# Performance work log

Hardware: AMD Instinct MI355X
Metric: run time of the kernel (lower is better)

The kernel has to match this reference:

```python
import jax, jax.numpy as jnp
import numpy as np

ALPHA = 30.0  # init kwarg alpha
K = 16        # init kwarg k


def setup_inputs() -> dict:
    key = jax.random.key(0)
    k1, k2 = jax.random.split(key)
    x = jax.random.normal(k1, (4096, 1024), dtype=jnp.float32)
    # L2-normalize embeddings (standard for metric-learning losses) so
    # pairwise distances lie in [0, 2] and exp(alpha*(1-d)) is well-scaled.
    x = x / jnp.linalg.norm(x, axis=1, keepdims=True)
    t = jax.random.randint(k2, (4096,), 0, 64)
    return {"inputs": x, "targets": t}


def _knn_softmax(inputs, targets):
    n = inputs.shape[0]
    # pairwise euclidean distances, clamp(1e-12).sqrt as in euclidean_dist
    sq = jnp.sum(inputs * inputs, axis=1)
    dist = sq[:, None] + sq[None, :] - 2.0 * (inputs @ inputs.T)
    dist = jnp.sqrt(jnp.clip(dist, 1e-12))  # [n, n]

    eye = jnp.eye(n, dtype=bool)
    same = targets[:, None] == targets[None, :]
    pos_mask = same & ~eye        # same label, off-diagonal
    neg_mask = ~same              # different label (diag excluded automatically)

    # threshold = (K+1)-th smallest off-diagonal distance per row
    # (equals sorted(concat(pos_pair, neg_pair))[K] in the original)
    BIG = jnp.float32(1e30)
    thr = jnp.sort(jnp.where(eye, BIG, dist), axis=1)[:, K]  # [n]

    below = dist < thr[:, None]
    logits = jnp.exp(ALPHA * (1.0 - dist))  # exp(alpha*(1 - d)) per pair

    pos_below = pos_mask & below
    neg_below = neg_mask & below
    pos_logit = jnp.sum(jnp.where(pos_below, logits, 0.0), axis=1)
    neg_logit = jnp.sum(jnp.where(neg_below, logits, 0.0), axis=1)

    # fallback: if no positive neighbor below threshold, use the first
    # positive pair (masked_select returns row order -> smallest index)
    first_pos = jnp.argmax(pos_mask, axis=1)
    fb = jnp.take_along_axis(logits, first_pos[:, None], axis=1)[:, 0]
    has_pos_below = jnp.any(pos_below, axis=1)
    pos_logit = jnp.where(has_pos_below, pos_logit, fb)

    loss_i = -jnp.log(pos_logit / (pos_logit + neg_logit))  # [n]

    # rows with no positive or no negative pair are skipped in the original
    valid = jnp.any(pos_mask, axis=1) & jnp.any(neg_mask, axis=1)
    n_valid = jnp.sum(valid.astype(jnp.float32))
    loss = jnp.sum(jnp.where(valid, loss_i, 0.0)) / n_valid
    accuracy = jnp.sum((valid & (loss_i < 0.6)).astype(jnp.float32)) / n
    return loss, accuracy


def reference(inputs, targets):
    loss, accuracy = _knn_softmax(inputs, targets)
    return (loss, accuracy, 0.0, 0.0)
```

## Files before the change

### kernel.cpp

```cpp
#include <hip/hip_runtime.h>
#include <hip/hip_bf16.h>
#include <cfloat>
#include <climits>
#include <cstdint>

#define ALPHA 30.0f
#define KSEL 16
#define P0 1.368f
#define P0SQ (P0 * P0)
#define CAP 224
#define TCAP 512
#define BIGV 1e30f
#define NMAX 4096

typedef __attribute__((ext_vector_type(4))) float f32x4;
typedef __attribute__((ext_vector_type(8))) int i32x8;
typedef __attribute__((ext_vector_type(4))) int i32x4;

#define LDS_PTR(p) ((__attribute__((address_space(3))) uint32_t*)(p))
#define GLB_PTR(p) ((const __attribute__((address_space(1))) uint32_t*)(p))

__device__ inline float bfval(ushort u) {
    return __builtin_bit_cast(float, (uint32_t)u << 16);
}

__device__ inline float blockReduceSumF(float v, float* s) {
    for (int off = 32; off; off >>= 1) v += __shfl_down(v, off);
    int tid = threadIdx.x, wid = tid >> 6;
    if ((tid & 63) == 0) s[wid] = v;
    __syncthreads();
    float r;
    if (tid == 0) { r = s[0] + s[1] + s[2] + s[3]; s[0] = r; }
    __syncthreads();
    r = s[0];
    __syncthreads();
    return r;
}

__device__ inline int blockReduceSumI(int v, int* s) {
    for (int off = 32; off; off >>= 1) v += __shfl_down(v, off);
    int tid = threadIdx.x, wid = tid >> 6;
    if ((tid & 63) == 0) s[wid] = v;
    __syncthreads();
    int r;
    if (tid == 0) { r = s[0] + s[1] + s[2] + s[3]; s[0] = r; }
    __syncthreads();
    r = s[0];
    __syncthreads();
    return r;
}

__device__ inline int blockReduceMaxI(int v, int* s) {
    for (int off = 32; off; off >>= 1) v = max(v, __shfl_down(v, off));
    int tid = threadIdx.x, wid = tid >> 6;
    if ((tid & 63) == 0) s[wid] = v;
    __syncthreads();
    int r;
    if (tid == 0) { r = max(max(s[0], s[1]), max(s[2], s[3])); s[0] = r; }
    __syncthreads();
    r = s[0];
    __syncthreads();
    return r;
}

__global__ __launch_bounds__(256) void prep_kernel(const float* __restrict__ X,
                                                   ushort* __restrict__ Xbf,
                                                   uint32_t* __restrict__ Xb8,
                                                   float* __restrict__ sq,
                                                   const int* __restrict__ targets,
                                                   int* __restrict__ f1,
                                                   int* __restrict__ f2,
                                                   int* __restrict__ lcnt,
                                                   int* __restrict__ cntArr,
                                                   int* __restrict__ needFB,
                                                   int D, int N) {
    __shared__ float sw[4];
    __shared__ int s1[4], s2[4], sc[4];
    int tid = threadIdx.x;
    int wid = tid >> 6;

    if (blockIdx.x >= (unsigned)N) {
        int lbl = blockIdx.x - N;
        int a1 = INT_MAX, a2 = INT_MAX, c = 0;
        for (int j = tid; j < N; j += 256) {
            if (targets[j] == lbl) {
                ++c;
                if (j < a1) { a2 = a1; a1 = j; }
                else if (j < a2) a2 = j;
            }
        }
        for (int off = 32; off; off >>= 1) {
            int b1 = __shfl_down(a1, off), b2 = __shfl_down(a2, off), bc = __shfl_down(c, off);
            int m1 = min(a1, b1);
            int m2 = min(max(a1, b1), min(a2, b2));
            a1 = m1; a2 = m2; c += bc;
        }
        if ((tid & 63) == 0) { s1[wid] = a1; s2[wid] = a2; sc[wid] = c; }
        __syncthreads();
        if (tid == 0) {
            int r1 = s1[0], r2 = s2[0], rc = sc[0];
            for (int w = 1; w < 4; ++w) {
                int m1 = min(r1, s1[w]);
                int m2 = min(max(r1, s1[w]), min(r2, s2[w]));
                r1 = m1; r2 = m2; rc += sc[w];
            }
            f1[lbl] = r1; f2[lbl] = r2; lcnt[lbl] = rc;
        }
        return;
    }

    int row = blockIdx.x;
    if (tid == 0) { cntArr[row] = 0; needFB[row] = 0; }
    const float4* xr = reinterpret_cast<const float4*>(X + (size_t)row * D);
    ushort4* xo = reinterpret_cast<ushort4*>(Xbf + (size_t)row * D);
    uint32_t* x8o = Xb8 + (size_t)row * (D / 4);
    float s = 0.f;
    for (int c = tid; c < D / 4; c += 256) {
        float4 v = xr[c];
        s += v.x * v.x + v.y * v.y + v.z * v.z + v.w * v.w;
        ushort4 o;
        uint32_t b;
        b = __builtin_bit_cast(uint32_t, v.x); o.x = (ushort)((b + 0x7FFF + ((b >> 16) & 1)) >> 16);
        b = __builtin_bit_cast(uint32_t, v.y); o.y = (ushort)((b + 0x7FFF + ((b >> 16) & 1)) >> 16);
        b = __builtin_bit_cast(uint32_t, v.z); o.z = (ushort)((b + 0x7FFF + ((b >> 16) & 1)) >> 16);
        b = __builtin_bit_cast(uint32_t, v.w); o.w = (ushort)((b + 0x7FFF + ((b >> 16) & 1)) >> 16);
        xo[c] = o;
        int pk = __builtin_amdgcn_cvt_pk_fp8_f32(v.x * 16.f, v.y * 16.f, 0, false);
        pk = __builtin_amdgcn_cvt_pk_fp8_f32(v.z * 16.f, v.w * 16.f, pk, true);
        x8o[c] = (uint32_t)pk;
    }
    for (int off = 32; off; off >>= 1) s += __shfl_down(s, off);
    if ((tid & 63) == 0) sw[wid] = s;
    __syncthreads();
    if (tid == 0) sq[row] = sw[0] + sw[1] + sw[2] + sw[3];
}

#define GBM 128
#define GBK 128
__global__ __launch_bounds__(256) void distgemm_mfma(const uint8_t* __restrict__ Xb8,
                                                     const float* __restrict__ sq,
                                                     float2* __restrict__ cand,
                                                     int* __restrict__ cntArr,
                                                     int* __restrict__ needFB,
                                                     int N, int D) {
    if (blockIdx.x < blockIdx.y) return;
    __shared__ uint8_t As[GBM * GBK];
    __shared__ uint8_t Bs[GBM * GBK];
    __shared__ float2 tlist[TCAP];
    __shared__ int s_cnt;

    int by = blockIdx.y, bx = blockIdx.x;
    bool diag = (bx == by);

    int tid = threadIdx.x;
    int lane = tid & 63;
    int wave = tid >> 6;
    int waveR = wave >> 1;
    int waveC = wave & 1;

    int rowBase = by * GBM;
    int colBase = bx * GBM;

    if (tid == 0) s_cnt = 0;

    f32x4 acc[4][4];
#pragma unroll
    for (int m = 0; m < 4; ++m)
#pragma unroll
        for (int n2 = 0; n2 < 4; ++n2) {
            f32x4 z = {0.f, 0.f, 0.f, 0.f};
            acc[m][n2] = z;
        }

    int srow = lane >> 3;
    int sgb = ((lane & 7) << 4) ^ (srow << 4);
    auto STAGE = [&](int k0) {
#pragma unroll
        for (int p = 0; p < 4; ++p) {
            int c = wave * 4 + p;
            int r = c * 8 + srow;
            const uint8_t* gA = Xb8 + (size_t)(rowBase + r) * D + k0 + sgb;
            const uint8_t* gB = Xb8 + (size_t)(colBase + r) * D + k0 + sgb;
            __builtin_amdgcn_global_load_lds(GLB_PTR(gA), LDS_PTR(&As[c * 1024]), 16, 0, 0);
            __builtin_amdgcn_global_load_lds(GLB_PTR(gB), LDS_PTR(&Bs[c * 1024]), 16, 0, 0);
        }
    };

    int l15 = lane & 15;
    int kq32 = (lane >> 4) * 32;
    int rswz = (l15 & 7) << 4;
    int nt = D / GBK;

    for (int t = 0; t < nt; ++t) {
        STAGE(t * GBK);
        __syncthreads();

        i32x8 bF[4];
#pragma unroll
        for (int n2 = 0; n2 < 4; ++n2) {
            int brl = waveC * 64 + n2 * 16 + l15;
            const uint8_t* base = Bs + brl * 128;
            i32x4 lo = *reinterpret_cast<const i32x4*>(base + ((kq32) ^ rswz));
            i32x4 hi = *reinterpret_cast<const i32x4*>(base + ((kq32 + 16) ^ rswz));
            i32x8 f = {lo[0], lo[1], lo[2], lo[3], hi[0], hi[1], hi[2], hi[3]};
            bF[n2] = f;
        }
        __builtin_amdgcn_s_setprio(1);
#pragma unroll
        for (int m = 0; m < 4; ++m) {
            int arl = waveR * 64 + m * 16 + l15;
            const uint8_t* base = As + arl * 128;
            i32x4 lo = *reinterpret_cast<const i32x4*>(base + ((kq32) ^ rswz));
            i32x4 hi = *reinterpret_cast<const i32x4*>(base + ((kq32 + 16) ^ rswz));
            i32x8 aF = {lo[0], lo[1], lo[2], lo[3], hi[0], hi[1], hi[2], hi[3]};
#pragma unroll
            for (int n2 = 0; n2 < 4; ++n2)
                acc[m][n2] = __builtin_amdgcn_mfma_scale_f32_16x16x128_f8f6f4(
                    aF, bF[n2], acc[m][n2], 0, 0, 0, 0x7F, 0, 0x7F);
        }
        __builtin_amdgcn_s_setprio(0);
        __syncthreads();
    }

    int cr = (lane >> 4) * 4;
    int cc = lane & 15;
    unsigned long long lmask_lt = (1ull << lane) - 1ull;
#pragma unroll
    for (int m = 0; m < 4; ++m) {
#pragma unroll
        for (int n2 = 0; n2 < 4; ++n2) {
            int gcol = colBase + waveC * 64 + n2 * 16 + cc;
            float sqc = sq[gcol];
#pragma unroll
            for (int r = 0; r < 4; ++r) {
                int grow = rowBase + waveR * 64 + m * 16 + cr + r;
                float v = sq[grow] + sqc - acc[m][n2][r] * 0.0078125f;
                bool pred = (v < P0SQ) && (grow != gcol);
                unsigned long long mask = __ballot(pred);
                if (mask) {
                    int leader = __ffsll((long long)mask) - 1;
                    int tot = __popcll(mask);
                    int base = 0;
                    if (lane == leader) base = atomicAdd(&s_cnt, tot);
                    base = __shfl(base, leader);
                    if (pred) {
                        int idx = base + __popcll(mask & lmask_lt);
                        if (idx < TCAP) {
                            float d = sqrtf(fmaxf(v, 1e-12f));
                            uint32_t pk = ((uint32_t)grow << 12) | (uint32_t)gcol;
                            float2 e; e.x = d; e.y = __builtin_bit_cast(float, pk);
                            tlist[idx] = e;
                        }
                    }
                }
            }
        }
    }
    __syncthreads();

    int cnt = min(s_cnt, TCAP);
    for (int e = tid; e < cnt; e += 256) {
        float2 v = tlist[e];
        uint32_t pk = __builtin_bit_cast(uint32_t, v.y);
        int i = (int)(pk >> 12), j = (int)(pk & 4095u);
        int p = atomicAdd(&cntArr[i], 1);
        if (p < CAP) {
            float2 e1; e1.x = v.x; e1.y = __builtin_bit_cast(float, j);
            cand[(size_t)i * CAP + p] = e1;
        }
        if (!diag) {
            int q = atomicAdd(&cntArr[j], 1);
            if (q < CAP) {
                float2 e2; e2.x = v.x; e2.y = __builtin_bit_cast(float, i);
                cand[(size_t)j * CAP + q] = e2;
            }
        }
    }
    if (s_cnt > TCAP) {
        if (tid < GBM) needFB[rowBase + tid] = 1;
        else needFB[colBase + tid - GBM] = 1;
    }
}

__global__ __launch_bounds__(256) void rowfinal_kernel(const float2* __restrict__ cand,
                                                       const int* __restrict__ cntArr,
                                                       const int* __restrict__ targets,
                                                       const ushort* __restrict__ Xbf,
                                                       const float* __restrict__ sq,
                                                       const int* __restrict__ f1,
                                                       const int* __restrict__ f2,
                                                       const int* __restrict__ lcnt,
                                                       int* __restrict__ needFB,
                                                       float* __restrict__ rowLoss,
                                                       int N, int D) {
    __shared__ float dbuf[4][CAP];
    int tid = threadIdx.x, lane = tid & 63, w = tid >> 6;
    int row = blockIdx.x * 4 + w;
    int ti = targets[row];
    int lc = lcnt[ti];
    bool validRow = (lc >= 2) && (lc < N);
    int cnt = cntArr[row];
    bool fb = (cnt < KSEL + 1) || (cnt > CAP);
    int lim = fb ? 0 : cnt;

    float ed[4]; int ej[4];
#pragma unroll
    for (int s = 0; s < 4; ++s) {
        int idx = lane + s * 64;
        bool in = (!fb) && (idx < cnt);
        if (in) {
            float2 e = cand[(size_t)row * CAP + idx];
            ed[s] = e.x; ej[s] = __builtin_bit_cast(int, e.y);
            dbuf[w][idx] = e.x;
        } else { ed[s] = BIGV; ej[s] = -1; }
    }
    __syncthreads();

    int rlo[4] = {0, 0, 0, 0}, req[4] = {0, 0, 0, 0};
    for (int q = 0; q < lim; ++q) {
        float u = dbuf[w][q];
#pragma unroll
        for (int s = 0; s < 4; ++s) {
            rlo[s] += (u < ed[s]);
            req[s] += (u == ed[s]);
        }
    }
    float thrc = BIGV;
#pragma unroll
    for (int s = 0; s < 4; ++s)
        if (ej[s] >= 0 && rlo[s] <= KSEL && KSEL < rlo[s] + req[s]) thrc = fminf(thrc, ed[s]);
    for (int off = 32; off; off >>= 1) thrc = fminf(thrc, __shfl_down(thrc, off));
    float thr = __shfl(thrc, 0);

    float posS = 0.f, negS = 0.f;
    int apb = 0;
#pragma unroll
    for (int s = 0; s < 4; ++s) {
        if (ej[s] >= 0 && ed[s] < thr) {
            bool same = (targets[ej[s]] == ti);
            float e = expf(ALPHA * (1.0f - ed[s]));
            if (same) { posS += e; apb = 1; }
            else negS += e;
        }
    }
    for (int off = 32; off; off >>= 1) {
        posS += __shfl_down(posS, off);
        negS += __shfl_down(negS, off);
        apb = max(apb, __shfl_down(apb, off));
    }

    int fp = 0;
    float dot = 0.f;
    if (validRow) {
        fp = (row == f1[ti]) ? f2[ti] : f1[ti];
        const ushort* xr = Xbf + (size_t)row * D;
        const ushort* xf = Xbf + (size_t)fp * D;
        for (int c = lane; c < D / 4; c += 64) {
            ushort4 a = *reinterpret_cast<const ushort4*>(xr + (size_t)c * 4);
            ushort4 b = *reinterpret_cast<const ushort4*>(xf + (size_t)c * 4);
            dot += bfval(a.x) * bfval(b.x) + bfval(a.y) * bfval(b.y)
                 + bfval(a.z) * bfval(b.z) + bfval(a.w) * bfval(b.w);
        }
    }
    for (int off = 32; off; off >>= 1) dot += __shfl_down(dot, off);

    if (lane == 0) {
        if (fb) {
            needFB[row] = 1;
        } else if (!validRow) {
            rowLoss[row] = BIGV;
        } else {
            float fbD = sqrtf(fmaxf(sq[row] + sq[fp] - 2.0f * dot, 1e-12f));
            float posLogit = apb ? posS : expf(ALPHA * (1.0f - fbD));
            rowLoss[row] = -logf(posLogit / (posLogit + negS));
        }
    }
}

__global__ __launch_bounds__(256) void fallback_kernel(const ushort* __restrict__ Xbf,
                                                       const float* __restrict__ sq,
                                                       const int* __restrict__ targets,
                                                       const int* __restrict__ needFB,
                                                       const int* __restrict__ f1,
                                                       const int* __restrict__ f2,
                                                       const int* __restrict__ lcnt,
                                                       float* __restrict__ rowLoss,
                                                       int N, int D) {
    int row = blockIdx.x;
    if (!needFB[row]) return;

    __shared__ float xrow[1024];
    __shared__ float rowD[NMAX];
    __shared__ float sF[4];
    __shared__ int sI[4];
    int tid = threadIdx.x;

    for (int k = tid; k < D; k += 256) xrow[k] = bfval(Xbf[(size_t)row * D + k]);
    __syncthreads();

    for (int j = tid; j < N; j += 256) {
        float dot = 0.f;
        const ushort* xj = Xbf + (size_t)j * D;
        for (int k = 0; k < D; ++k) dot += xrow[k] * bfval(xj[k]);
        rowD[j] = (j == row) ? BIGV
                             : sqrtf(fmaxf(sq[row] + sq[j] - 2.0f * dot, 1e-12f));
    }
    __syncthreads();

    uint32_t lo = 0, hi = 0x40800000u;
    while (lo < hi) {
        uint32_t mid = (lo + hi) >> 1;
        float mv = __builtin_bit_cast(float, mid);
        int c = 0;
        for (int j = tid; j < N; j += 256) c += (rowD[j] <= mv);
        c = blockReduceSumI(c, sI);
        if (c >= KSEL + 1) hi = mid; else lo = mid + 1;
    }
    float thr = __builtin_bit_cast(float, hi);

    int ti = targets[row];
    int lc = lcnt[ti];
    bool validRow = (lc >= 2) && (lc < N);

    float posS = 0.f, negS = 0.f;
    int apb = 0;
    for (int j = tid; j < N; j += 256) {
        if (j == row) continue;
        float d = rowD[j];
        bool same = (targets[j] == ti);
        if (d < thr) {
            float e = expf(ALPHA * (1.0f - d));
            if (same) { posS += e; apb = 1; }
            else negS += e;
        }
    }
    posS = blockReduceSumF(posS, sF);
    negS = blockReduceSumF(negS, sF);
    apb = blockReduceMaxI(apb, sI);

    if (tid == 0) {
        if (!validRow) { rowLoss[row] = BIGV; return; }
        int fp = (row == f1[ti]) ? f2[ti] : f1[ti];
        float posLogit = apb ? posS : expf(ALPHA * (1.0f - rowD[fp]));
        rowLoss[row] = -logf(posLogit / (posLogit + negS));
    }
}

__global__ __launch_bounds__(256) void reduce_kernel(const float* __restrict__ rowLoss,
                                                     float* __restrict__ out, int N) {
    __shared__ float sF[4];
    __shared__ int sI[4];
    int tid = threadIdx.x;
    float sumL = 0.f;
    int nValid = 0, nAcc = 0;
    for (int j = tid; j < N; j += 256) {
        float L = rowLoss[j];
        if (L != BIGV) {
            sumL += L;
            ++nValid;
            if (L < 0.6f) ++nAcc;
        }
    }
    sumL = blockReduceSumF(sumL, sF);
    nValid = blockReduceSumI(nValid, sI);
    nAcc = blockReduceSumI(nAcc, sI);
    if (tid == 0) {
        out[0] = (nValid > 0) ? sumL / (float)nValid : 0.f;
        out[1] = (float)nAcc / (float)N;
        out[2] = 0.f;
        out[3] = 0.f;
    }
}

extern "C" void kernel_launch(void* const* d_in, const int* in_sizes, int n_in,
                              void* d_out, int out_size, void* d_ws, size_t ws_size,
                              hipStream_t stream) {
    const float* X = (const float*)d_in[0];
    const int* targets = (const int*)d_in[1];
    float* out = (float*)d_out;

    int N = in_sizes[1];
    int D = in_sizes[0] / N;
    int tiles = N / GBM;

    float2* cand     = (float2*)d_ws;
    float*  sq       = (float*)(cand + (size_t)N * CAP);
    float*  rowLoss  = sq + N;
    int*    cntArr   = (int*)(rowLoss + N);
    int*    needFB   = cntArr + N;
    int*    f1       = needFB + N;
    int*    f2       = f1 + 64;
    int*    lcnt     = f2 + 64;
    ushort* Xbf      = (ushort*)(lcnt + 64 + 64);
    uint32_t* Xb8    = (uint32_t*)(Xbf + (size_t)N * D);

    prep_kernel<<<N + 64, 256, 0, stream>>>(X, Xbf, Xb8, sq, targets,
                                            f1, f2, lcnt, cntArr, needFB, D, N);

    dim3 grid(tiles, tiles);
    distgemm_mfma<<<grid, 256, 0, stream>>>((const uint8_t*)Xb8, sq, cand,
                                            cntArr, needFB, N, D);

    rowfinal_kernel<<<N / 4, 256, 0, stream>>>(cand, cntArr, targets, Xbf, sq,
                                               f1, f2, lcnt, needFB, rowLoss, N, D);

    fallback_kernel<<<N, 256, 0, stream>>>(Xbf, sq, targets, needFB,
                                           f1, f2, lcnt, rowLoss, N, D);

    reduce_kernel<<<1, 256, 0, stream>>>(rowLoss, out, N);
}
```

Baseline: 108.9 us.

## Load FP8 GEMM fragments directly from global memory, bypassing LDS staging

```diff
diff --git a/kernel.cpp b/kernel.cpp
--- a/kernel.cpp
+++ b/kernel.cpp
@@ -16,9 +16,6 @@
 typedef __attribute__((ext_vector_type(4))) float f32x4;
 typedef __attribute__((ext_vector_type(8))) int i32x8;
 typedef __attribute__((ext_vector_type(4))) int i32x4;
-
-#define LDS_PTR(p) ((__attribute__((address_space(3))) uint32_t*)(p))
-#define GLB_PTR(p) ((const __attribute__((address_space(1))) uint32_t*)(p))
 
 __device__ inline float bfval(ushort u) {
     return __builtin_bit_cast(float, (uint32_t)u << 16);
@@ -144,8 +141,6 @@
                                                      int* __restrict__ needFB,
                                                      int N, int D) {
     if (blockIdx.x < blockIdx.y) return;
-    __shared__ uint8_t As[GBM * GBK];
-    __shared__ uint8_t Bs[GBM * GBK];
     __shared__ float2 tlist[TCAP];
     __shared__ int s_cnt;
 
@@ -172,55 +167,48 @@
             acc[m][n2] = z;
         }
 
-    int srow = lane >> 3;
-    int sgb = ((lane & 7) << 4) ^ (srow << 4);
-    auto STAGE = [&](int k0) {
-#pragma unroll
-        for (int p = 0; p < 4; ++p) {
-            int c = wave * 4 + p;
-            int r = c * 8 + srow;
-            const uint8_t* gA = Xb8 + (size_t)(rowBase + r) * D + k0 + sgb;
-            const uint8_t* gB = Xb8 + (size_t)(colBase + r) * D + k0 + sgb;
-            __builtin_amdgcn_global_load_lds(GLB_PTR(gA), LDS_PTR(&As[c * 1024]), 16, 0, 0);
-            __builtin_amdgcn_global_load_lds(GLB_PTR(gB), LDS_PTR(&Bs[c * 1024]), 16, 0, 0);
-        }
-    };
-
     int l15 = lane & 15;
     int kq32 = (lane >> 4) * 32;
-    int rswz = (l15 & 7) << 4;
+    const uint8_t* aRow[4];
+    const uint8_t* bRow[4];
+#pragma unroll
+    for (int m = 0; m < 4; ++m) {
+        aRow[m] = Xb8 + (size_t)(rowBase + waveR * 64 + m * 16 + l15) * D + kq32;
+        bRow[m] = Xb8 + (size_t)(colBase + waveC * 64 + m * 16 + l15) * D + kq32;
+    }
+
     int nt = D / GBK;
-
     for (int t = 0; t < nt; ++t) {
-        STAGE(t * GBK);
-        __syncthreads();
-
-        i32x8 bF[4];
-#pragma unroll
-        for (int n2 = 0; n2 < 4; ++n2) {
-            int brl = waveC * 64 + n2 * 16 + l15;
-            const uint8_t* base = Bs + brl * 128;
-            i32x4 lo = *reinterpret_cast<const i32x4*>(base + ((kq32) ^ rswz));
-            i32x4 hi = *reinterpret_cast<const i32x4*>(base + ((kq32 + 16) ^ rswz));
-            i32x8 f = {lo[0], lo[1], lo[2], lo[3], hi[0], hi[1], hi[2], hi[3]};
-            bF[n2] = f;
+        int k0 = t * GBK;
+        i32x4 alo[4], ahi[4], blo[4], bhi[4];
+#pragma unroll
+        for (int m = 0; m < 4; ++m) {
+            alo[m] = *reinterpret_cast<const i32x4*>(aRow[m] + k0);
+            ahi[m] = *reinterpret_cast<const i32x4*>(aRow[m] + k0 + 16);
+            blo[m] = *reinterpret_cast<const i32x4*>(bRow[m] + k0);
+            bhi[m] = *reinterpret_cast<const i32x4*>(bRow[m] + k0 + 16);
+        }
+        i32x8 aF[4], bF[4];
+#pragma unroll
+        for (int m = 0; m < 4; ++m) {
+            i32x8 fa = {alo[m][0], alo[m][1], alo[m][2], alo[m][3],
+                        ahi[m][0], ahi[m][1], ahi[m][2], ahi[m][3]};
+            aF[m] = fa;
+            i32x8 fb = {blo[m][0], blo[m][1], blo[m][2], blo[m][3],
+                        bhi[m][0], bhi[m][1], bhi[m][2], bhi[m][3]};
+            bF[m] = fb;
         }
         __builtin_amdgcn_s_setprio(1);
 #pragma unroll
-        for (int m = 0; m < 4; ++m) {
-            int arl = waveR * 64 + m * 16 + l15;
-            const uint8_t* base = As + arl * 128;
-            i32x4 lo = *reinterpret_cast<const i32x4*>(base + ((kq32) ^ rswz));
-            i32x4 hi = *reinterpret_cast<const i32x4*>(base + ((kq32 + 16) ^ rswz));
-            i32x8 aF = {lo[0], lo[1], lo[2], lo[3], hi[0], hi[1], hi[2], hi[3]};
+        for (int m = 0; m < 4; ++m)
 #pragma unroll
             for (int n2 = 0; n2 < 4; ++n2)
                 acc[m][n2] = __builtin_amdgcn_mfma_scale_f32_16x16x128_f8f6f4(
-                    aF, bF[n2], acc[m][n2], 0, 0, 0, 0x7F, 0, 0x7F);
-        }
+                    aF[m], bF[n2], acc[m][n2], 0, 0, 0, 0x7F, 0, 0x7F);
         __builtin_amdgcn_s_setprio(0);
-        __syncthreads();
-    }
+    }
+
+    __syncthreads();
 
     int cr = (lane >> 4) * 4;
     int cc = lane & 15;
```

After: 144.5 us. +32.7%, slower.
